# Kernel optimization log

Measured on AMD Instinct MI355X. Metric: run time of the kernel, lower is better.

## Reference

```python
import jax, jax.numpy as jnp
import numpy as np

NEG_BIG = -9e15  # matches torch's -9000000000000000.0 mask value
ALPHA = 0.2      # LeakyReLU negative slope


def setup_inputs() -> dict:
    key = jax.random.key(0)
    k1, k2, k3 = jax.random.split(key, 3)
    B, N, Fin, Fout = 8, 2048, 64, 64
    h = jax.random.normal(k1, (B, N, Fin), dtype=jnp.float32)
    adj = jax.random.randint(k2, (B, N, N), 0, 2, dtype=jnp.int32)
    kW, ka = jax.random.split(k3)
    # xavier_uniform with gain=1.414
    gW = 1.414 * np.sqrt(6.0 / (Fin + Fout))
    W = jax.random.uniform(kW, (Fin, Fout), minval=-gW, maxval=gW, dtype=jnp.float32)
    ga = 1.414 * np.sqrt(6.0 / (2 * Fout + 1))
    a = jax.random.uniform(ka, (2 * Fout, 1), minval=-ga, maxval=ga, dtype=jnp.float32)
    return {"h": h, "adj": adj, "W": W, "a": a}


def reference(h, adj, W, a):
    # Wh: [B, N, Fout]
    Wh = jnp.einsum("bnf,fo->bno", h, W)
    Fout = W.shape[1]
    a1 = a[:Fout, 0]   # source part of attention vector
    a2 = a[Fout:, 0]   # target part
    # e_ij = leakyrelu(a1.Wh_i + a2.Wh_j) -- rank-1 decomposition of the
    # repeat/cat construction; avoids the [B,N,N,2F] intermediate.
    s = Wh @ a1        # [B, N]
    t = Wh @ a2        # [B, N]
    e = s[:, :, None] + t[:, None, :]            # [B, N, N]
    e = jnp.where(e > 0, e, ALPHA * e)           # LeakyReLU
    e = jnp.where(adj > 0, e, NEG_BIG)           # adjacency mask
    attention = jax.nn.softmax(e, axis=2)
    # dropout omitted: reference is eval-mode (F.dropout is identity when not training)
    h_prime = jnp.einsum("bij,bjo->bio", attention, Wh)
    return jax.nn.elu(h_prime)                   # concat=True branch
```

## Files before the change

### kernel.cpp

```cpp
#include <hip/hip_runtime.h>


#define ALPHA 0.2f

typedef __attribute__((ext_vector_type(8))) short  short8;
typedef __attribute__((ext_vector_type(4))) float  f32x4;

static __device__ __forceinline__ unsigned short f2bf(float f) {
    unsigned u = __builtin_bit_cast(unsigned, f);
    u += 0x7fffu + ((u >> 16) & 1u);
    return (unsigned short)(u >> 16);
}

static __device__ __forceinline__ unsigned pack_bf2(float lo, float hi) {
    unsigned ulo = __builtin_bit_cast(unsigned, lo) + 0x8000u;
    unsigned uhi = __builtin_bit_cast(unsigned, hi) + 0x8000u;
    return __builtin_amdgcn_perm(uhi, ulo, 0x07060302);
}

__global__ __launch_bounds__(256) void k01(
    const float* __restrict__ h, const int* __restrict__ adj,
    const float* __restrict__ W, const float* __restrict__ a,
    uint4* __restrict__ whF, float* __restrict__ sw,
    float* __restrict__ tw, unsigned char* __restrict__ mask)
{
    __shared__ float W_l[64 * 65];
    __shared__ float wa[128];
    __shared__ float tile[4 * 16 * 65];

    const int tid = threadIdx.x;

    if (blockIdx.x >= 256) {
        const int mb = blockIdx.x - 256;
        const int4* a4 = (const int4*)adj;
        #pragma unroll 1
        for (int g0 = 0; g0 < 16; g0 += 4) {
            int4 v0a, v0b, v1a, v1b, v2a, v2b, v3a, v3b;
            const size_t p0 = (size_t)mb * 4096 + (size_t)g0 * 256 + tid;
            v0a = a4[p0 * 2];          v0b = a4[p0 * 2 + 1];
            v1a = a4[(p0 + 256) * 2];  v1b = a4[(p0 + 256) * 2 + 1];
            v2a = a4[(p0 + 512) * 2];  v2b = a4[(p0 + 512) * 2 + 1];
            v3a = a4[(p0 + 768) * 2];  v3b = a4[(p0 + 768) * 2 + 1];
            unsigned b0 = (v0a.x ? 1u:0u)|(v0a.y ? 2u:0u)|(v0a.z ? 4u:0u)|(v0a.w ? 8u:0u)
                        | (v0b.x ?16u:0u)|(v0b.y ?32u:0u)|(v0b.z ?64u:0u)|(v0b.w ?128u:0u);
            unsigned b1 = (v1a.x ? 1u:0u)|(v1a.y ? 2u:0u)|(v1a.z ? 4u:0u)|(v1a.w ? 8u:0u)
                        | (v1b.x ?16u:0u)|(v1b.y ?32u:0u)|(v1b.z ?64u:0u)|(v1b.w ?128u:0u);
            unsigned b2 = (v2a.x ? 1u:0u)|(v2a.y ? 2u:0u)|(v2a.z ? 4u:0u)|(v2a.w ? 8u:0u)
                        | (v2b.x ?16u:0u)|(v2b.y ?32u:0u)|(v2b.z ?64u:0u)|(v2b.w ?128u:0u);
            unsigned b3 = (v3a.x ? 1u:0u)|(v3a.y ? 2u:0u)|(v3a.z ? 4u:0u)|(v3a.w ? 8u:0u)
                        | (v3b.x ?16u:0u)|(v3b.y ?32u:0u)|(v3b.z ?64u:0u)|(v3b.w ?128u:0u);
            mask[p0]       = (unsigned char)b0;
            mask[p0 + 256] = (unsigned char)b1;
            mask[p0 + 512] = (unsigned char)b2;
            mask[p0 + 768] = (unsigned char)b3;
        }
        return;
    }

    const int lane = tid & 63, wv = tid >> 6;
    const int im   = lane & 15, kq = lane >> 4;

    #pragma unroll
    for (int k = 0; k < 16; ++k) {
        int e = tid + 256 * k;
        W_l[(e >> 6) * 65 + (e & 63)] = W[e];
    }
    __syncthreads();

    if (tid < 128) {
        int f = tid & 63;
        const float* ap = a + (tid >> 6) * 64;
        float acc = 0.f;
        #pragma unroll 8
        for (int o = 0; o < 64; ++o) acc += W_l[f * 65 + o] * ap[o];
        wa[tid] = acc;
    }
    __syncthreads();

    short8 bf[4][2];
    #pragma unroll
    for (int nb = 0; nb < 4; ++nb)
        #pragma unroll
        for (int ks = 0; ks < 2; ++ks)
            #pragma unroll
            for (int u = 0; u < 8; ++u)
                bf[nb][ks][u] = (short)f2bf(W_l[(ks * 32 + kq * 8 + u) * 65 + nb * 16 + im]);

    const int row0 = blockIdx.x * 64 + wv * 16;
    const float* hrow = h + (size_t)(row0 + im) * 64;

    float hv[2][8];
    short8 af[2];
    float sp = 0.f, tp = 0.f;
    #pragma unroll
    for (int ks = 0; ks < 2; ++ks) {
        float4 A = *(const float4*)(hrow + ks * 32 + kq * 8);
        float4 Bv = *(const float4*)(hrow + ks * 32 + kq * 8 + 4);
        hv[ks][0] = A.x;  hv[ks][1] = A.y;  hv[ks][2] = A.z;  hv[ks][3] = A.w;
        hv[ks][4] = Bv.x; hv[ks][5] = Bv.y; hv[ks][6] = Bv.z; hv[ks][7] = Bv.w;
        #pragma unroll
        for (int u = 0; u < 8; ++u) {
            int f = ks * 32 + kq * 8 + u;
            sp += hv[ks][u] * wa[f];
            tp += hv[ks][u] * wa[64 + f];
            af[ks][u] = (short)f2bf(hv[ks][u]);
        }
    }
    sp += __shfl_xor(sp, 16, 64); sp += __shfl_xor(sp, 32, 64);
    tp += __shfl_xor(tp, 16, 64); tp += __shfl_xor(tp, 32, 64);
    if (lane < 16) {
        sw[row0 + lane] = sp;
        tw[row0 + lane] = tp;
    }

    f32x4 acc[4] = {{0.f,0.f,0.f,0.f},{0.f,0.f,0.f,0.f},{0.f,0.f,0.f,0.f},{0.f,0.f,0.f,0.f}};
    #pragma unroll
    for (int ks = 0; ks < 2; ++ks)
        #pragma unroll
        for (int nb = 0; nb < 4; ++nb)
            acc[nb] = __builtin_amdgcn_mfma_f32_16x16x32_bf16(af[ks], bf[nb][ks], acc[nb], 0, 0, 0);

    #pragma unroll
    for (int nb = 0; nb < 4; ++nb)
        #pragma unroll
        for (int r = 0; r < 4; ++r)
            tile[wv * 1040 + (kq * 4 + r) * 65 + nb * 16 + im] = acc[nb][r];
    __syncthreads();

    {
        const int blk_row0 = blockIdx.x * 64;
        const int bb2 = blk_row0 >> 11;
        const int c_base = (blk_row0 & 2047) >> 5;
        #pragma unroll
        for (int k = 0; k < 2; ++k) {
            int e = tid + 256 * k;
            int l = e & 63, ot = (e >> 6) & 3, cl_ = e >> 8;
            int o = ot * 16 + (l & 15);
            int jb = cl_ * 32 + (l >> 4) * 8;
            unsigned d0, d1, d2, d3;
            {
                int j0 = jb;
                d0 = pack_bf2(tile[(j0 >> 4) * 1040 + (j0 & 15) * 65 + o],
                              tile[(j0 >> 4) * 1040 + ((j0 & 15) + 1) * 65 + o]);
                j0 = jb + 2;
                d1 = pack_bf2(tile[(j0 >> 4) * 1040 + (j0 & 15) * 65 + o],
                              tile[(j0 >> 4) * 1040 + ((j0 & 15) + 1) * 65 + o]);
                j0 = jb + 4;
                d2 = pack_bf2(tile[(j0 >> 4) * 1040 + (j0 & 15) * 65 + o],
                              tile[(j0 >> 4) * 1040 + ((j0 & 15) + 1) * 65 + o]);
                j0 = jb + 6;
                d3 = pack_bf2(tile[(j0 >> 4) * 1040 + (j0 & 15) * 65 + o],
                              tile[(j0 >> 4) * 1040 + ((j0 & 15) + 1) * 65 + o]);
            }
            uint4 val = {d0, d1, d2, d3};
            whF[(size_t)(((bb2 * 64 + c_base + cl_) * 4 + ot)) * 64 + l] = val;
        }
    }
}

__global__ __launch_bounds__(256, 4) void k2_attn(
    const unsigned* __restrict__ mask, const uint4* __restrict__ whF,
    const float* __restrict__ sw, const float* __restrict__ tw,
    float* __restrict__ out)
{
    __shared__ float eB[2048];
    __shared__ float eD[2048];
    __shared__ float cpart[4 * 1040];
    __shared__ float zp[64];

    const int tid  = threadIdx.x;
    const int lane = tid & 63, wv = tid >> 6;
    const int im   = lane & 15, kq = lane >> 4;
    const int b    = blockIdx.x >> 7;
    const int i0   = (blockIdx.x & 127) << 4;

    {
        const float4* tp4 = (const float4*)(tw + (size_t)b * 2048);
        float4 t0 = tp4[tid], t1 = tp4[tid + 256];
        float4 e0 = {__expf(t0.x), __expf(t0.y), __expf(t0.z), __expf(t0.w)};
        float4 e1 = {__expf(t1.x), __expf(t1.y), __expf(t1.z), __expf(t1.w)};
        float4 f0 = {__expf(ALPHA*t0.x), __expf(ALPHA*t0.y), __expf(ALPHA*t0.z), __expf(ALPHA*t0.w)};
        float4 f1 = {__expf(ALPHA*t1.x), __expf(ALPHA*t1.y), __expf(ALPHA*t1.z), __expf(ALPHA*t1.w)};
        *(float4*)&eB[tid * 4] = e0;  *(float4*)&eB[(tid + 256) * 4] = e1;
        *(float4*)&eD[tid * 4] = f0;  *(float4*)&eD[(tid + 256) * 4] = f1;
    }

    const uint4* mrow4 = (const uint4*)(mask + (size_t)(b * 2048 + i0 + im) * 64 + wv * 16);
    const uint4 mA = mrow4[0], mB = mrow4[1], mC = mrow4[2], mD = mrow4[3];
    const unsigned mm[16] = {mA.x, mA.y, mA.z, mA.w, mB.x, mB.y, mB.z, mB.w,
                             mC.x, mC.y, mC.z, mC.w, mD.x, mD.y, mD.z, mD.w};

    const float sl = sw[b * 2048 + i0 + im];
    const float al = __expf(sl), cl_ = __expf(ALPHA * sl);
    const int j00 = wv * 512 + kq * 8;
    const uint4* wbase = whF + (size_t)((b * 64 + wv * 16) * 4) * 64 + lane;

    short8 ones;
    #pragma unroll
    for (int u = 0; u < 8; ++u) ones[u] = (short)0x3F80;

    __syncthreads();

    f32x4 acc0 = {0.f,0.f,0.f,0.f}, acc1 = {0.f,0.f,0.f,0.f};
    f32x4 acc2 = {0.f,0.f,0.f,0.f}, acc3 = {0.f,0.f,0.f,0.f};
    f32x4 accz = {0.f,0.f,0.f,0.f};

    uint4 c0 = wbase[0], c1 = wbase[64], c2 = wbase[128], c3 = wbase[192];

    #pragma unroll
    for (int s = 0; s < 16; ++s) {
        uint4 n0, n1, n2, n3;
        if (s < 15) {
            n0 = wbase[(s + 1) * 256      ];
            n1 = wbase[(s + 1) * 256 +  64];
            n2 = wbase[(s + 1) * 256 + 128];
            n3 = wbase[(s + 1) * 256 + 192];
        } else {
            n0 = c0; n1 = c1; n2 = c2; n3 = c3;
        }

        const float4 bA  = *(const float4*)&eB[j00 + s * 32];
        const float4 bBv = *(const float4*)&eB[j00 + s * 32 + 4];
        const float4 dA  = *(const float4*)&eD[j00 + s * 32];
        const float4 dBv = *(const float4*)&eD[j00 + s * 32 + 4];
        const unsigned mbyte = (mm[s] >> (kq * 8)) & 0xffu;

        float p0 = fmaxf(al * bA.x,  cl_ * dA.x);   p0 = (mbyte &   1u) ? p0 : 0.f;
        float p1 = fmaxf(al * bA.y,  cl_ * dA.y);   p1 = (mbyte &   2u) ? p1 : 0.f;
        float p2 = fmaxf(al * bA.z,  cl_ * dA.z);   p2 = (mbyte &   4u) ? p2 : 0.f;
        float p3 = fmaxf(al * bA.w,  cl_ * dA.w);   p3 = (mbyte &   8u) ? p3 : 0.f;
        float p4 = fmaxf(al * bBv.x, cl_ * dBv.x);  p4 = (mbyte &  16u) ? p4 : 0.f;
        float p5 = fmaxf(al * bBv.y, cl_ * dBv.y);  p5 = (mbyte &  32u) ? p5 : 0.f;
        float p6 = fmaxf(al * bBv.z, cl_ * dBv.z);  p6 = (mbyte &  64u) ? p6 : 0.f;
        float p7 = fmaxf(al * bBv.w, cl_ * dBv.w);  p7 = (mbyte & 128u) ? p7 : 0.f;

        int4 ai;
        ai.x = (int)pack_bf2(p0, p1);
        ai.y = (int)pack_bf2(p2, p3);
        ai.z = (int)pack_bf2(p4, p5);
        ai.w = (int)pack_bf2(p6, p7);
        const short8 af = __builtin_bit_cast(short8, ai);

        acc0 = __builtin_amdgcn_mfma_f32_16x16x32_bf16(af, __builtin_bit_cast(short8, c0), acc0, 0, 0, 0);
        acc1 = __builtin_amdgcn_mfma_f32_16x16x32_bf16(af, __builtin_bit_cast(short8, c1), acc1, 0, 0, 0);
        acc2 = __builtin_amdgcn_mfma_f32_16x16x32_bf16(af, __builtin_bit_cast(short8, c2), acc2, 0, 0, 0);
        acc3 = __builtin_amdgcn_mfma_f32_16x16x32_bf16(af, __builtin_bit_cast(short8, c3), acc3, 0, 0, 0);
        accz = __builtin_amdgcn_mfma_f32_16x16x32_bf16(af, ones, accz, 0, 0, 0);

        c0 = n0; c1 = n1; c2 = n2; c3 = n3;
    }

    if (im == 0) {
        #pragma unroll
        for (int r = 0; r < 4; ++r) zp[wv * 16 + kq * 4 + r] = accz[r];
    }

    #pragma unroll
    for (int r = 0; r < 4; ++r) {
        cpart[wv * 1040 + (kq * 4 + r) * 65 +  0 + im] = acc0[r];
        cpart[wv * 1040 + (kq * 4 + r) * 65 + 16 + im] = acc1[r];
        cpart[wv * 1040 + (kq * 4 + r) * 65 + 32 + im] = acc2[r];
        cpart[wv * 1040 + (kq * 4 + r) * 65 + 48 + im] = acc3[r];
    }
    __syncthreads();

    #pragma unroll
    for (int k = 0; k < 4; ++k) {
        int idx = tid + 256 * k;
        int i = idx >> 6, o = idx & 63;
        float ssum = cpart[0 * 1040 + i * 65 + o] + cpart[1 * 1040 + i * 65 + o]
                   + cpart[2 * 1040 + i * 65 + o] + cpart[3 * 1040 + i * 65 + o];
        float z = zp[i] + zp[16 + i] + zp[32 + i] + zp[48 + i];
        if (z == 0.f) z = 1.f;
        float r = ssum / z;
        out[((size_t)(b * 2048 + i0 + i)) * 64 + o] = r > 0.f ? r : expm1f(r);
    }
}

extern "C" void kernel_launch(void* const* d_in, const int* in_sizes, int n_in,
                              void* d_out, int out_size, void* d_ws, size_t ws_size,
                              hipStream_t stream) {
    const float* h   = (const float*)d_in[0];
    const int*   adj = (const int*)d_in[1];
    const float* W   = (const float*)d_in[2];
    const float* a   = (const float*)d_in[3];
    float* out = (float*)d_out;

    uint4* whF = (uint4*)d_ws;
    float* sw  = (float*)((char*)d_ws + 2097152);
    float* tw  = (float*)((char*)d_ws + 2097152 + 65536);
    unsigned char* mask = (unsigned char*)((char*)d_ws + 2097152 + 131072);

    hipLaunchKernelGGL(k01, dim3(1280), dim3(256), 0, stream, h, adj, W, a, whF, sw, tw, mask);
    hipLaunchKernelGGL(k2_attn, dim3(1024), dim3(256), 0, stream,
                       (const unsigned*)mask, whF, sw, tw, out);
}
```

Baseline: 215.6 us.

## Fuse adjacency bitmask packing into attention kernel via shared memory

The adjacency-to-bitmask packing moves out of the first kernel and into the attention kernel. Each attention block now reads its own 16 rows of int adjacency, packs them into 32-bit words in shared memory, and the lanes read their mask words from there. This drops the global mask write and re-read and shrinks the first kernel's grid. In exchange the attention kernel takes on the full adjacency read at its start, uses more LDS per block (which may reduce occupancy), and serialises that read before compute.

```diff
diff --git a/kernel.cpp b/kernel.cpp
--- a/kernel.cpp
+++ b/kernel.cpp
@@ -18,45 +18,21 @@
     return __builtin_amdgcn_perm(uhi, ulo, 0x07060302);
 }
 
-__global__ __launch_bounds__(256) void k01(
-    const float* __restrict__ h, const int* __restrict__ adj,
-    const float* __restrict__ W, const float* __restrict__ a,
-    uint4* __restrict__ whF, float* __restrict__ sw,
-    float* __restrict__ tw, unsigned char* __restrict__ mask)
+static __device__ __forceinline__ unsigned nib4(int4 v) {
+    return (v.x != 0 ? 1u : 0u) | (v.y != 0 ? 2u : 0u)
+         | (v.z != 0 ? 4u : 0u) | (v.w != 0 ? 8u : 0u);
+}
+
+__global__ __launch_bounds__(256) void k1_wh_st(
+    const float* __restrict__ h, const float* __restrict__ W,
+    const float* __restrict__ a, uint4* __restrict__ whF,
+    float* __restrict__ sw, float* __restrict__ tw)
 {
     __shared__ float W_l[64 * 65];
     __shared__ float wa[128];
     __shared__ float tile[4 * 16 * 65];
 
-    const int tid = threadIdx.x;
-
-    if (blockIdx.x >= 256) {
-        const int mb = blockIdx.x - 256;
-        const int4* a4 = (const int4*)adj;
-        #pragma unroll 1
-        for (int g0 = 0; g0 < 16; g0 += 4) {
-            int4 v0a, v0b, v1a, v1b, v2a, v2b, v3a, v3b;
-            const size_t p0 = (size_t)mb * 4096 + (size_t)g0 * 256 + tid;
-            v0a = a4[p0 * 2];          v0b = a4[p0 * 2 + 1];
-            v1a = a4[(p0 + 256) * 2];  v1b = a4[(p0 + 256) * 2 + 1];
-            v2a = a4[(p0 + 512) * 2];  v2b = a4[(p0 + 512) * 2 + 1];
-            v3a = a4[(p0 + 768) * 2];  v3b = a4[(p0 + 768) * 2 + 1];
-            unsigned b0 = (v0a.x ? 1u:0u)|(v0a.y ? 2u:0u)|(v0a.z ? 4u:0u)|(v0a.w ? 8u:0u)
-                        | (v0b.x ?16u:0u)|(v0b.y ?32u:0u)|(v0b.z ?64u:0u)|(v0b.w ?128u:0u);
-            unsigned b1 = (v1a.x ? 1u:0u)|(v1a.y ? 2u:0u)|(v1a.z ? 4u:0u)|(v1a.w ? 8u:0u)
-                        | (v1b.x ?16u:0u)|(v1b.y ?32u:0u)|(v1b.z ?64u:0u)|(v1b.w ?128u:0u);
-            unsigned b2 = (v2a.x ? 1u:0u)|(v2a.y ? 2u:0u)|(v2a.z ? 4u:0u)|(v2a.w ? 8u:0u)
-                        | (v2b.x ?16u:0u)|(v2b.y ?32u:0u)|(v2b.z ?64u:0u)|(v2b.w ?128u:0u);
-            unsigned b3 = (v3a.x ? 1u:0u)|(v3a.y ? 2u:0u)|(v3a.z ? 4u:0u)|(v3a.w ? 8u:0u)
-                        | (v3b.x ?16u:0u)|(v3b.y ?32u:0u)|(v3b.z ?64u:0u)|(v3b.w ?128u:0u);
-            mask[p0]       = (unsigned char)b0;
-            mask[p0 + 256] = (unsigned char)b1;
-            mask[p0 + 512] = (unsigned char)b2;
-            mask[p0 + 768] = (unsigned char)b3;
-        }
-        return;
-    }
-
+    const int tid  = threadIdx.x;
     const int lane = tid & 63, wv = tid >> 6;
     const int im   = lane & 15, kq = lane >> 4;
 
@@ -159,12 +135,13 @@
 }
 
 __global__ __launch_bounds__(256, 4) void k2_attn(
-    const unsigned* __restrict__ mask, const uint4* __restrict__ whF,
+    const int* __restrict__ adj, const uint4* __restrict__ whF,
     const float* __restrict__ sw, const float* __restrict__ tw,
     float* __restrict__ out)
 {
     __shared__ float eB[2048];
     __shared__ float eD[2048];
+    __shared__ unsigned mask_l[16 * 65];
     __shared__ float cpart[4 * 1040];
     __shared__ float zp[64];
 
@@ -173,6 +150,21 @@
     const int im   = lane & 15, kq = lane >> 4;
     const int b    = blockIdx.x >> 7;
     const int i0   = (blockIdx.x & 127) << 4;
+
+    {
+        const int* adjb = adj + (size_t)(b * 2048 + i0) * 2048;
+        #pragma unroll
+        for (int g = 0; g < 4; ++g) {
+            const int Wd = tid + g * 256;
+            const int r = Wd >> 6, wr = Wd & 63;
+            const int4* p = (const int4*)(adjb + (size_t)r * 2048 + wr * 32);
+            int4 v0 = p[0], v1 = p[1], v2 = p[2], v3 = p[3];
+            int4 v4 = p[4], v5 = p[5], v6 = p[6], v7 = p[7];
+            unsigned w = nib4(v0)        | (nib4(v1) << 4)  | (nib4(v2) << 8)  | (nib4(v3) << 12)
+                       | (nib4(v4) << 16)| (nib4(v5) << 20) | (nib4(v6) << 24) | (nib4(v7) << 28);
+            mask_l[r * 65 + wr] = w;
+        }
+    }
 
     {
         const float4* tp4 = (const float4*)(tw + (size_t)b * 2048);
@@ -185,11 +177,6 @@
         *(float4*)&eD[tid * 4] = f0;  *(float4*)&eD[(tid + 256) * 4] = f1;
     }
 
-    const uint4* mrow4 = (const uint4*)(mask + (size_t)(b * 2048 + i0 + im) * 64 + wv * 16);
-    const uint4 mA = mrow4[0], mB = mrow4[1], mC = mrow4[2], mD = mrow4[3];
-    const unsigned mm[16] = {mA.x, mA.y, mA.z, mA.w, mB.x, mB.y, mB.z, mB.w,
-                             mC.x, mC.y, mC.z, mC.w, mD.x, mD.y, mD.z, mD.w};
-
     const float sl = sw[b * 2048 + i0 + im];
     const float al = __expf(sl), cl_ = __expf(ALPHA * sl);
     const int j00 = wv * 512 + kq * 8;
@@ -200,6 +187,17 @@
     for (int u = 0; u < 8; ++u) ones[u] = (short)0x3F80;
 
     __syncthreads();
+
+    unsigned mm[16];
+    {
+        const unsigned* mrow = &mask_l[im * 65 + wv * 16];
+        #pragma unroll
+        for (int s4 = 0; s4 < 4; ++s4) {
+            uint4 m = *(const uint4*)(mrow + s4 * 4);
+            mm[s4 * 4 + 0] = m.x; mm[s4 * 4 + 1] = m.y;
+            mm[s4 * 4 + 2] = m.z; mm[s4 * 4 + 3] = m.w;
+        }
+    }
 
     f32x4 acc0 = {0.f,0.f,0.f,0.f}, acc1 = {0.f,0.f,0.f,0.f};
     f32x4 acc2 = {0.f,0.f,0.f,0.f}, acc3 = {0.f,0.f,0.f,0.f};
@@ -289,9 +287,7 @@
     uint4* whF = (uint4*)d_ws;
     float* sw  = (float*)((char*)d_ws + 2097152);
     float* tw  = (float*)((char*)d_ws + 2097152 + 65536);
-    unsigned char* mask = (unsigned char*)((char*)d_ws + 2097152 + 131072);
-
-    hipLaunchKernelGGL(k01, dim3(1280), dim3(256), 0, stream, h, adj, W, a, whF, sw, tw, mask);
-    hipLaunchKernelGGL(k2_attn, dim3(1024), dim3(256), 0, stream,
-                       (const unsigned*)mask, whF, sw, tw, out);
-}
+
+    hipLaunchKernelGGL(k1_wh_st, dim3(256), dim3(256), 0, stream, h, W, a, whF, sw, tw);
+    hipLaunchKernelGGL(k2_attn, dim3(1024), dim3(256), 0, stream, adj, whF, sw, tw, out);
+}
```

After: 218.4 us. Within noise of the previous version (+1.3%).
